# Kernel tuning notes

Measured on AMD Instinct MI355X. Metric: run time of the kernel, lower is better.

Reference implementation:

```python
import jax, jax.numpy as jnp
import numpy as np

B, C, H, W = 4, 256, 64, 64


def setup_inputs() -> dict:
    key = jax.random.key(0)
    k1, k2, k3, k4 = jax.random.split(key, 4)
    inp = jax.random.normal(k1, (B, C, H, W), dtype=jnp.float32)
    inter_mask = jnp.ones((B, 1, H, W), dtype=jnp.float32)
    flow_init = jax.random.normal(k2, (B, 2, H, W), dtype=jnp.float32)
    # nn.Linear(C, C): weight [out,in], bias [out]
    lim = 1.0 / np.sqrt(C)
    W_lin = jax.random.uniform(k3, (C, C), dtype=jnp.float32, minval=-lim, maxval=lim)
    b_lin = jax.random.uniform(k4, (C,), dtype=jnp.float32, minval=-lim, maxval=lim)
    return {"inp": inp, "inter_mask": inter_mask, "flow_init": flow_init,
            "W_lin": W_lin, "b_lin": b_lin}


def reference(inp, inter_mask, flow_init, W_lin, b_lin):
    batch, ch, ht, wd = inp.shape
    n = ht * wd
    # [B, N, C]
    x = inp.reshape(batch, ch, n).transpose(0, 2, 1)
    x = x @ W_lin.T + b_lin
    scale = ch ** (-0.5)
    # [B, N, N] full self-correlation
    scores = jnp.einsum('bnc,bmc->bnm', x * scale, x)
    attn = jax.nn.softmax(scores, axis=-1)
    # [B, N, 2]
    flow = flow_init.reshape(batch, 2, n).transpose(0, 2, 1)
    flow_add = attn @ flow
    # [B, 2, H, W]
    return flow_add.reshape(batch, ht, wd, 2).transpose(0, 3, 1, 2)
```

## Files before the change

kernel.cpp:

```cpp
#include <hip/hip_runtime.h>
#include <hip/hip_bf16.h>

#define NB 4
#define CCH 256
#define NN 4096
#define QT 128
#define KSPLIT 4
#define MRANGE (NN / KSPLIT)
#define MTILE 64
#define NTILES (MRANGE / MTILE)

#define SQRTK 0.30028060f

typedef __attribute__((ext_vector_type(8))) short short8;
typedef __attribute__((ext_vector_type(16))) float f32x16;

__device__ inline ushort f2bf(float f) {
    uint u = __float_as_uint(f);
    uint r = (u + 0x7fffu + ((u >> 16) & 1u)) >> 16;
    return (ushort)r;
}

__device__ inline float dev_exp2(float x) {
#if __has_builtin(__builtin_amdgcn_exp2f)
    return __builtin_amdgcn_exp2f(x);
#else
    return exp2f(x);
#endif
}

__device__ inline void gl_lds16(const void* g, void* l) {
    __builtin_amdgcn_global_load_lds(
        (const __attribute__((address_space(1))) unsigned int*)g,
        (__attribute__((address_space(3))) unsigned int*)l, 16, 0, 0);
}

__global__ __launch_bounds__(256) void transp_k(const float* __restrict__ inp,
                                                ushort* __restrict__ inpT,
                                                const float* __restrict__ W,
                                                ushort* __restrict__ Wb) {
    if (blockIdx.x >= 1024) {
        int i = (blockIdx.x - 1024) * 256 + threadIdx.x;
        float4 v = reinterpret_cast<const float4*>(W)[i];
        ushort4 r;
        r.x = f2bf(v.x); r.y = f2bf(v.y); r.z = f2bf(v.z); r.w = f2bf(v.w);
        reinterpret_cast<ushort4*>(Wb)[i] = r;
        return;
    }
    int wg = blockIdx.x;
    int nblk = wg & 63, cblk = (wg >> 6) & 3, b = wg >> 8;
    __shared__ float tile[64 * 67];
    int t = threadIdx.x;
    const float* src = inp + ((size_t)(b * CCH + cblk * 64)) * NN + nblk * 64;
#pragma unroll
    for (int p = 0; p < 4; p++) {
        int ci = p * 256 + t;
        int c = ci >> 4, n4 = ci & 15;
        float4 v = *reinterpret_cast<const float4*>(src + (size_t)c * NN + n4 * 4);
        float* d = &tile[c * 67 + n4 * 4];
        d[0] = v.x; d[1] = v.y; d[2] = v.z; d[3] = v.w;
    }
    __syncthreads();
    ushort* dst = inpT + ((size_t)(b * NN + nblk * 64)) * CCH + cblk * 64;
#pragma unroll
    for (int p = 0; p < 2; p++) {
        int u = p * 256 + t;
        int n = u >> 3, cc = u & 7;
        ushort tmp[8];
#pragma unroll
        for (int j = 0; j < 8; j++) tmp[j] = f2bf(tile[(cc * 8 + j) * 67 + n]);
        uint4 o;
        o.x = (uint)tmp[0] | ((uint)tmp[1] << 16);
        o.y = (uint)tmp[2] | ((uint)tmp[3] << 16);
        o.z = (uint)tmp[4] | ((uint)tmp[5] << 16);
        o.w = (uint)tmp[6] | ((uint)tmp[7] << 16);
        *reinterpret_cast<uint4*>(dst + (size_t)n * CCH + cc * 8) = o;
    }
}

__global__ __launch_bounds__(256) void linear_k(const ushort* __restrict__ inpT,
                                                const ushort* __restrict__ Wb,
                                                const float* __restrict__ bias,
                                                ushort* __restrict__ xs) {
    int wg = blockIdx.x;
    int b = wg >> 6, nt = wg & 63;
    int t = threadIdx.x, l = t & 63, w = t >> 6;
    int nbase = nt * 64 + (w & 1) * 32;
    int obase = (w >> 1) * 128;
    const ushort* arow = inpT + ((size_t)(b * NN + nbase + (l & 31))) * CCH + ((l >> 5) * 8);
    const ushort* wrow = Wb + ((size_t)(obase + (l & 31))) * CCH + ((l >> 5) * 8);
    f32x16 acc[4];
#pragma unroll
    for (int os = 0; os < 4; os++)
#pragma unroll
        for (int r = 0; r < 16; r++) acc[os][r] = 0.f;

#pragma unroll
    for (int ch = 0; ch < 16; ch++) {
        short8 a = *reinterpret_cast<const short8*>(arow + ch * 16);
#pragma unroll
        for (int os = 0; os < 4; os++) {
            short8 bb = *reinterpret_cast<const short8*>(wrow + (size_t)os * 32 * CCH + ch * 16);
            acc[os] = __builtin_amdgcn_mfma_f32_32x32x16_bf16(a, bb, acc[os], 0, 0, 0);
        }
    }
#pragma unroll
    for (int os = 0; os < 4; os++) {
        int oc = obase + os * 32 + (l & 31);
        float bv = bias[oc];
#pragma unroll
        for (int r = 0; r < 16; r++) {
            int row = (r & 3) + 8 * (r >> 2) + 4 * (l >> 5);
            float v = (acc[os][r] + bv) * SQRTK;
            xs[((size_t)(b * NN + nt * 64 + (w & 1) * 32 + row)) * CCH + oc] = f2bf(v);
        }
    }
}

__global__ __launch_bounds__(256) void attn_k(const ushort* __restrict__ xs,
                                              const float* __restrict__ flow,
                                              float* __restrict__ part) {
    int wg = blockIdx.x;
    int b = wg >> 7;
    int qt = (wg >> 2) & 31;
    int ks = wg & 3;
    int t = threadIdx.x, l = t & 63, w = t >> 6;
    const ushort* xb = xs + (size_t)b * NN * CCH;
    int qbase = qt * QT + w * 32;
    int mstart = ks * MRANGE;

    short8 qf[16];
    const ushort* qrow = xb + ((size_t)(qbase + (l & 31))) * CCH + (l >> 5) * 8;
#pragma unroll
    for (int ch = 0; ch < 16; ch++)
        qf[ch] = *reinterpret_cast<const short8*>(qrow + ch * 16);

    __shared__ ushort kt[2][MTILE * 256];

    float accS[16], accX[16], accY[16];
#pragma unroll
    for (int r = 0; r < 16; r++) { accS[r] = 0.f; accX[r] = 0.f; accY[r] = 0.f; }

    auto stage = [&](int buf, int tile) {
        int mb = mstart + tile * MTILE;
        const char* src = (const char*)(xb + (size_t)mb * CCH);
#pragma unroll
        for (int p = 0; p < 8; p++) {
            int chunk = w * 8 + p;
            int lin = chunk * 1024 + l * 16;
            int row = lin >> 9;
            int cb = lin & 511;
            int gsw = cb ^ ((row & 15) << 4);
            gl_lds16(src + (size_t)row * 512 + gsw, &kt[buf][chunk * 512]);
        }
    };

    stage(0, 0);
    __syncthreads();
    int cur = 0;
    for (int tile = 0; tile < NTILES; tile++) {
        if (tile + 1 < NTILES) stage(cur ^ 1, tile + 1);
        int mb = mstart + tile * MTILE;
#pragma unroll
        for (int ms = 0; ms < 2; ms++) {
            f32x16 S;
#pragma unroll
            for (int r = 0; r < 16; r++) S[r] = 0.f;
            const char* base = (const char*)&kt[cur][(ms * 32 + (l & 31)) * 256];
            int swz = (l & 15) << 4;
#pragma unroll
            for (int ch = 0; ch < 16; ch++) {
                int cbyte = (ch * 32 + ((l >> 5) * 16)) ^ swz;
                short8 bf = *reinterpret_cast<const short8*>(base + cbyte);
                S = __builtin_amdgcn_mfma_f32_32x32x16_bf16(qf[ch], bf, S, 0, 0, 0);
            }
            int m = mb + ms * 32 + (l & 31);
            float fx = flow[(size_t)b * 2 * NN + m];
            float fy = flow[(size_t)b * 2 * NN + NN + m];
#pragma unroll
            for (int r = 0; r < 16; r++) {
                float e = dev_exp2(S[r]);
                accS[r] += e;
                accX[r] += e * fx;
                accY[r] += e * fy;
            }
        }
        __syncthreads();
        cur ^= 1;
    }

#pragma unroll
    for (int r = 0; r < 16; r++) {
        float s = accS[r], x = accX[r], y = accY[r];
#pragma unroll
        for (int off = 1; off < 32; off <<= 1) {
            s += __shfl_xor(s, off, 64);
            x += __shfl_xor(x, off, 64);
            y += __shfl_xor(y, off, 64);
        }
        if ((l & 31) == 0) {
            int row = (r & 3) + 8 * (r >> 2) + 4 * (l >> 5);
            int q = qt * QT + w * 32 + row;
            float* pb = part + ((size_t)(b * KSPLIT + ks)) * 3 * NN;
            pb[q] = s;
            pb[NN + q] = x;
            pb[2 * NN + q] = y;
        }
    }
}

__global__ void finalize_k(const float* __restrict__ part, float* __restrict__ out) {
    int i = blockIdx.x * 256 + threadIdx.x;
    int b = i >> 12, n = i & 4095;
    float s = 0.f, x = 0.f, y = 0.f;
#pragma unroll
    for (int ks = 0; ks < KSPLIT; ks++) {
        const float* p = part + ((size_t)(b * KSPLIT + ks)) * 3 * NN;
        s += p[n];
        x += p[NN + n];
        y += p[2 * NN + n];
    }
    out[(size_t)b * 2 * NN + n] = x / s;
    out[(size_t)b * 2 * NN + NN + n] = y / s;
}

extern "C" void kernel_launch(void* const* d_in, const int* in_sizes, int n_in,
                              void* d_out, int out_size, void* d_ws, size_t ws_size,
                              hipStream_t stream) {
    const float* inp  = (const float*)d_in[0];
    const float* flow = (const float*)d_in[2];
    const float* W    = (const float*)d_in[3];
    const float* bias = (const float*)d_in[4];
    float* out = (float*)d_out;

    char* ws = (char*)d_ws;
    ushort* xs   = (ushort*)(ws);
    ushort* inpT = (ushort*)(ws + 8388608);
    ushort* Wb   = (ushort*)(ws + 16777216);
    float*  part = (float*)(ws + 8388608);

    transp_k<<<1088, 256, 0, stream>>>(inp, inpT, W, Wb);
    linear_k<<<256, 256, 0, stream>>>(inpT, Wb, bias, xs);
    attn_k<<<512, 256, 0, stream>>>(xs, flow, part);
    finalize_k<<<64, 256, 0, stream>>>(part, out);
}
```

Baseline: 71.17 us.

## Compute attention-times-flow reduction with MFMA instead of scalar accumulation

The exp-weighted sums (denominator, flow x, flow y) were accumulated per element in VALU registers and then reduced with 32-lane shuffles. They are now computed by a second bf16 MFMA that multiplies the exponentiated scores by a small LDS-resident value matrix holding flow x, flow y, a ones column and zero padding. The QK product is transposed (K as the A operand) so the score layout matches the P operand of the PV MFMA. This removes the per-element FMAs and the final shuffle reduction, but rounds the probabilities and flow values to bf16 and uses most of the 32 value columns as zero padding.

```diff
diff --git a/kernel.cpp b/kernel.cpp
--- a/kernel.cpp
+++ b/kernel.cpp
@@ -9,11 +9,13 @@
 #define MRANGE (NN / KSPLIT)
 #define MTILE 64
 #define NTILES (MRANGE / MTILE)
+#define VPAD 8
 
 #define SQRTK 0.30028060f
 
 typedef __attribute__((ext_vector_type(8))) short short8;
 typedef __attribute__((ext_vector_type(16))) float f32x16;
+typedef __attribute__((ext_vector_type(4))) int i32x4;
 
 __device__ inline ushort f2bf(float f) {
     uint u = __float_as_uint(f);
@@ -129,17 +131,35 @@
     int qbase = qt * QT + w * 32;
     int mstart = ks * MRANGE;
 
+    __shared__ ushort kt[2][MTILE * 256];
+    __shared__ ushort vlds[4][MRANGE + VPAD];
+
+    {
+        int m0 = t * 4;
+        float4 fx4 = *reinterpret_cast<const float4*>(flow + (size_t)b * 2 * NN + mstart + m0);
+        float4 fy4 = *reinterpret_cast<const float4*>(flow + (size_t)b * 2 * NN + NN + mstart + m0);
+        float fxv[4] = {fx4.x, fx4.y, fx4.z, fx4.w};
+        float fyv[4] = {fy4.x, fy4.y, fy4.z, fy4.w};
+#pragma unroll
+        for (int i = 0; i < 4; i++) {
+            int m = m0 + i, ml = m & 15;
+            int pos = (m & ~15) | (ml & 3) | ((ml & 4) << 1) | ((ml & 8) >> 1);
+            vlds[0][pos] = f2bf(fxv[i]);
+            vlds[1][pos] = f2bf(fyv[i]);
+            vlds[2][pos] = 0x3F80;
+            vlds[3][pos] = 0;
+        }
+    }
+
     short8 qf[16];
     const ushort* qrow = xb + ((size_t)(qbase + (l & 31))) * CCH + (l >> 5) * 8;
 #pragma unroll
     for (int ch = 0; ch < 16; ch++)
         qf[ch] = *reinterpret_cast<const short8*>(qrow + ch * 16);
 
-    __shared__ ushort kt[2][MTILE * 256];
-
-    float accS[16], accX[16], accY[16];
-#pragma unroll
-    for (int r = 0; r < 16; r++) { accS[r] = 0.f; accX[r] = 0.f; accY[r] = 0.f; }
+    f32x16 pv;
+#pragma unroll
+    for (int r = 0; r < 16; r++) pv[r] = 0.f;
 
     auto stage = [&](int buf, int tile) {
         int mb = mstart + tile * MTILE;
@@ -155,12 +175,12 @@
         }
     };
 
+    int c_sel = (l & 31) < 3 ? (l & 31) : 3;
     stage(0, 0);
     __syncthreads();
     int cur = 0;
     for (int tile = 0; tile < NTILES; tile++) {
         if (tile + 1 < NTILES) stage(cur ^ 1, tile + 1);
-        int mb = mstart + tile * MTILE;
 #pragma unroll
         for (int ms = 0; ms < 2; ms++) {
             f32x16 S;
@@ -171,40 +191,40 @@
 #pragma unroll
             for (int ch = 0; ch < 16; ch++) {
                 int cbyte = (ch * 32 + ((l >> 5) * 16)) ^ swz;
-                short8 bf = *reinterpret_cast<const short8*>(base + cbyte);
-                S = __builtin_amdgcn_mfma_f32_32x32x16_bf16(qf[ch], bf, S, 0, 0, 0);
+                short8 kf = *reinterpret_cast<const short8*>(base + cbyte);
+                S = __builtin_amdgcn_mfma_f32_32x32x16_bf16(kf, qf[ch], S, 0, 0, 0);
             }
-            int m = mb + ms * 32 + (l & 31);
-            float fx = flow[(size_t)b * 2 * NN + m];
-            float fy = flow[(size_t)b * 2 * NN + NN + m];
-#pragma unroll
-            for (int r = 0; r < 16; r++) {
-                float e = dev_exp2(S[r]);
-                accS[r] += e;
-                accX[r] += e * fx;
-                accY[r] += e * fy;
+#pragma unroll
+            for (int r = 0; r < 16; r++) S[r] = dev_exp2(S[r]);
+            uint wd[8];
+#pragma unroll
+            for (int p = 0; p < 8; p++) {
+                float lo = S[2 * p], hi = S[2 * p + 1];
+                asm("v_cvt_pk_bf16_f32 %0, %1, %2" : "=v"(wd[p]) : "v"(lo), "v"(hi));
             }
+            i32x4 lo4 = {(int)wd[0], (int)wd[1], (int)wd[2], (int)wd[3]};
+            i32x4 hi4 = {(int)wd[4], (int)wd[5], (int)wd[6], (int)wd[7]};
+            short8 pa0 = __builtin_bit_cast(short8, lo4);
+            short8 pa1 = __builtin_bit_cast(short8, hi4);
+            int mloc = tile * MTILE + ms * 32;
+            const ushort* vb = &vlds[c_sel][mloc + (l >> 5) * 8];
+            short8 v0 = *reinterpret_cast<const short8*>(vb);
+            short8 v1 = *reinterpret_cast<const short8*>(vb + 16);
+            pv = __builtin_amdgcn_mfma_f32_32x32x16_bf16(pa0, v0, pv, 0, 0, 0);
+            pv = __builtin_amdgcn_mfma_f32_32x32x16_bf16(pa1, v1, pv, 0, 0, 0);
         }
         __syncthreads();
         cur ^= 1;
     }
 
-#pragma unroll
-    for (int r = 0; r < 16; r++) {
-        float s = accS[r], x = accX[r], y = accY[r];
-#pragma unroll
-        for (int off = 1; off < 32; off <<= 1) {
-            s += __shfl_xor(s, off, 64);
-            x += __shfl_xor(x, off, 64);
-            y += __shfl_xor(y, off, 64);
-        }
-        if ((l & 31) == 0) {
+    int c = l & 31;
+    if (c < 3) {
+        float* pb = part + ((size_t)(b * KSPLIT + ks)) * 3 * NN;
+        int off = ((c + 1) % 3) * NN;
+#pragma unroll
+        for (int r = 0; r < 16; r++) {
             int row = (r & 3) + 8 * (r >> 2) + 4 * (l >> 5);
-            int q = qt * QT + w * 32 + row;
-            float* pb = part + ((size_t)(b * KSPLIT + ks)) * 3 * NN;
-            pb[q] = s;
-            pb[NN + q] = x;
-            pb[2 * NN + q] = y;
+            pb[off + qbase + row] = pv[r];
         }
     }
 }
```

Result: faster. 65.79 us (-7.6%).
